# Optimization experiments

Hardware: AMD Instinct MI355X
Metric: run time of the kernel (lower is better)

Reference implementation:

```python
import jax, jax.numpy as jnp
import numpy as np

B, T, D, H = 4, 2048, 1024, 16
DH = D // H  # head dim = 64

def setup_inputs() -> dict:
    key = jax.random.key(0)
    k1, k2, k3, k4, k5, k6 = jax.random.split(key, 6)
    x = jax.random.normal(k1, (B, T, D), dtype=jnp.float32)
    mask = jax.random.randint(k2, (B, 1, 1, T), 0, 2, dtype=jnp.int32)
    # nn.Linear(out_dim, out_dim*3): weight stored here as [in, out]
    W_qkv = jax.random.normal(k3, (D, 3 * D), dtype=jnp.float32) * (1.0 / np.sqrt(D))
    b_qkv = jax.random.normal(k4, (3 * D,), dtype=jnp.float32) * 0.02
    W_out = jax.random.normal(k5, (D, D), dtype=jnp.float32) * (1.0 / np.sqrt(D))
    b_out = jax.random.normal(k6, (D,), dtype=jnp.float32) * 0.02
    return {"x": x, "mask": mask, "W_qkv": W_qkv, "b_qkv": b_qkv,
            "W_out": W_out, "b_out": b_out}

def reference(x, mask, W_qkv, b_qkv, W_out, b_out):
    # QKV projection: [B,T,3D]
    qkv = x @ W_qkv + b_qkv
    q, k, v = qkv[..., :D], qkv[..., D:2 * D], qkv[..., 2 * D:]
    # split heads -> [B,H,T,DH]
    def split(t):
        return t.reshape(B, T, H, DH).transpose(0, 2, 1, 3)
    q, k, v = split(q), split(k), split(v)
    # scaled dot-product attention (scale = sqrt(head_dim), per torch source)
    scores = jnp.einsum('bhqd,bhkd->bhqk', q, k) / jnp.sqrt(jnp.float32(DH))
    scores = jnp.where(mask == 0, jnp.float32(-1000.0), scores)
    weights = jax.nn.softmax(scores, axis=-1)  # dropout = identity (eval mode)
    out = jnp.einsum('bhqk,bhkd->bhqd', weights, v)
    out = out.transpose(0, 2, 1, 3).reshape(B, T, D)
    return out @ W_out + b_out
```

## Files before the change

### kernel.cpp

```cpp
#include <hip/hip_runtime.h>
#include <hip/hip_bf16.h>
#include <stdint.h>

#define B_  4
#define T_  2048
#define D_  1024
#define H_  16
#define DH_ 64

typedef _Float16 half8 __attribute__((ext_vector_type(8)));
typedef _Float16 half4 __attribute__((ext_vector_type(4)));
typedef __fp16   fp16x2 __attribute__((ext_vector_type(2)));
typedef float    f32x4 __attribute__((ext_vector_type(4)));

#define MFMA16(a, b, c) __builtin_amdgcn_mfma_f32_16x16x32_f16(a, b, c, 0, 0, 0)

__device__ static inline void gload_lds16(const void* g, void* l) {
  __builtin_amdgcn_global_load_lds(
      (const __attribute__((address_space(1))) void*)g,
      (__attribute__((address_space(3))) void*)l, 16, 0, 0);
}

__global__ __launch_bounds__(256)
void prep_all(const float* __restrict__ x, const int* __restrict__ mask,
              const float* __restrict__ wqkv, const float* __restrict__ wout,
              _Float16* __restrict__ xh, _Float16* __restrict__ mh,
              _Float16* __restrict__ wqkvt, _Float16* __restrict__ woutt) {
  __shared__ float tile[32][33];
  const int bid = blockIdx.x, t = threadIdx.x;
  if (bid < 2048) {
    const long n = (long)B_ * T_ * D_;
    long i = ((long)bid * 256 + t) * 4;
    const long stride = (long)2048 * 256 * 4;
    for (; i < n; i += stride) {
      float4 v = *(const float4*)(x + i);
      half4 hv;
      hv.x = (_Float16)v.x; hv.y = (_Float16)v.y; hv.z = (_Float16)v.z; hv.w = (_Float16)v.w;
      *(half4*)(xh + i) = hv;
    }
  } else if (bid < 6144) {
    const float* in;
    _Float16* out;
    int n0, k0, N;
    if (bid < 5120) {
      int id = bid - 2048;
      in = wqkv; out = wqkvt; N = 3 * D_;
      n0 = (id % 96) * 32; k0 = (id / 96) * 32;
    } else {
      int id = bid - 5120;
      in = wout; out = woutt; N = D_;
      n0 = (id % 32) * 32; k0 = (id / 32) * 32;
    }
    const int xx = t & 31, y = t >> 5;
    #pragma unroll
    for (int j = 0; j < 32; j += 8)
      tile[y + j][xx] = in[(long)(k0 + y + j) * N + n0 + xx];
    __syncthreads();
    #pragma unroll
    for (int j = 0; j < 32; j += 8)
      out[(long)(n0 + y + j) * D_ + k0 + xx] = (_Float16)tile[xx][y + j];
  } else {
    int i = (bid - 6144) * 256 + t;
    mh[i] = mask[i] ? (_Float16)1.0f : (_Float16)0.0f;
  }
}

template <int EPI>
__global__ __launch_bounds__(256, 2)
void mha_gemm2(const _Float16* __restrict__ A, const _Float16* __restrict__ Bt,
               const float* __restrict__ bias, const _Float16* __restrict__ mhp,
               _Float16* __restrict__ qo, _Float16* __restrict__ ko, _Float16* __restrict__ vo,
               float* __restrict__ co, int M, int N, int K, int gx) {
  __shared__ _Float16 shbuf[16384];
  _Float16* const As = shbuf;
  _Float16* const Bs = shbuf + 8192;
  const int t = threadIdx.x;
  const int l = t & 63;
  const int w = t >> 6;
  const int wr = w >> 1, wc = w & 1;

  const int cpx = gridDim.x >> 3;
  const int wg = (blockIdx.x & 7) * cpx + (blockIdx.x >> 3);
  const int m0 = (wg / gx) * 128, n0 = (wg % gx) * 128;

  const _Float16* ag[4];
  const _Float16* bg[4];
  #pragma unroll
  for (int j = 0; j < 4; ++j) {
    int c = j * 256 + t;
    int row = c >> 3, sub = c & 7;
    int s = (sub ^ (row & 7)) * 8;
    ag[j] = A  + (long)(m0 + row) * K + s;
    bg[j] = Bt + (long)(n0 + row) * K + s;
  }

  f32x4 acc[4][4];
  #pragma unroll
  for (int f = 0; f < 4; ++f)
    #pragma unroll
    for (int g = 0; g < 4; ++g) acc[f][g] = (f32x4){0.f, 0.f, 0.f, 0.f};

  const int hi = l >> 4;

  for (int k0 = 0; k0 < K; k0 += 64) {
    #pragma unroll
    for (int j = 0; j < 4; ++j) {
      gload_lds16(ag[j] + k0, &As[j * 2048 + w * 512]);
      gload_lds16(bg[j] + k0, &Bs[j * 2048 + w * 512]);
    }
    __syncthreads();
    half8 af[2][4], bf[2][4];
    #pragma unroll
    for (int kk = 0; kk < 2; ++kk)
      #pragma unroll
      for (int f = 0; f < 4; ++f) {
        int ra = wr * 64 + f * 16 + (l & 15);
        int rb = wc * 64 + f * 16 + (l & 15);
        af[kk][f] = *(const half8*)((const char*)As + ra * 128 +
                                    ((((kk << 2) | hi) ^ (ra & 7)) << 4));
        bf[kk][f] = *(const half8*)((const char*)Bs + rb * 128 +
                                    ((((kk << 2) | hi) ^ (rb & 7)) << 4));
      }
    #pragma unroll
    for (int kk = 0; kk < 2; ++kk)
      #pragma unroll
      for (int f = 0; f < 4; ++f)
        #pragma unroll
        for (int g = 0; g < 4; ++g)
          acc[f][g] = MFMA16(af[kk][f], bf[kk][g], acc[f][g]);
    __syncthreads();
  }

  if constexpr (EPI == 0) {
    if (n0 >= 2 * D_) {
      const int bb = m0 >> 11, m0t = m0 & 2047;
      #pragma unroll
      for (int g = 0; g < 4; ++g) {
        int colL = wc * 64 + g * 16 + (l & 15);
        float bv = bias[n0 + colL];
        int swz = (colL & 7) << 4;
        #pragma unroll
        for (int f = 0; f < 4; ++f) {
          int row0 = wr * 64 + f * 16 + hi * 4;
          half4 hv;
          #pragma unroll
          for (int r = 0; r < 4; ++r) {
            float mv = (float)mhp[bb * T_ + m0t + row0 + r];
            hv[r] = (_Float16)((acc[f][g][r] + bv) * mv);
          }
          *(half4*)&shbuf[colL * 128 + (row0 ^ swz)] = hv;
        }
      }
      __syncthreads();
      #pragma unroll
      for (int i = 0; i < 8; ++i) {
        int e = i * 256 + t;
        int colL = e >> 4, chunk = e & 15;
        int swz = (colL & 7) << 4;
        half8 v8 = *(const half8*)&shbuf[colL * 128 + ((chunk * 8) ^ swz)];
        int d = (n0 + colL) & 1023;
        int h2 = d >> 6, dh = d & 63;
        *(half8*)&vo[(((long)bb * H_ + h2) * DH_ + dh) * T_ + m0t + chunk * 8] = v8;
      }
    } else {
      #pragma unroll
      for (int g = 0; g < 4; ++g) {
        int j = n0 + wc * 64 + g * 16 + (l & 15);
        float bv = bias[j];
        int which = j >> 10;
        int d = j & 1023;
        int h = d >> 6, dh = d & 63;
        _Float16* base = which == 0 ? qo : ko;
        float sc = which == 0 ? 0.1803368801f : 1.0f;
        #pragma unroll
        for (int f = 0; f < 4; ++f) {
          int row0 = m0 + wr * 64 + f * 16 + ((l >> 4) << 2);
          #pragma unroll
          for (int r = 0; r < 4; ++r) {
            int row = row0 + r;
            int bb = row >> 11, tt = row & 2047;
            base[(((long)bb * H_ + h) * T_ + tt) * DH_ + dh] =
                (_Float16)((acc[f][g][r] + bv) * sc);
          }
        }
      }
    }
  } else {
    #pragma unroll
    for (int g = 0; g < 4; ++g) {
      int j = n0 + wc * 64 + g * 16 + (l & 15);
      float bv = bias[j];
      #pragma unroll
      for (int f = 0; f < 4; ++f) {
        int row0 = m0 + wr * 64 + f * 16 + ((l >> 4) << 2);
        #pragma unroll
        for (int r = 0; r < 4; ++r)
          co[(long)(row0 + r) * N + j] = acc[f][g][r] + bv;
      }
    }
  }
}

__global__ __launch_bounds__(128, 2)
void mha_attn7(const _Float16* __restrict__ Q, const _Float16* __restrict__ K,
               const _Float16* __restrict__ Vt, const _Float16* __restrict__ mh,
               _Float16* __restrict__ out) {
  __shared__ _Float16 Ksh[2][4096];
  __shared__ _Float16 Vsh[2][4096];
  const int t = threadIdx.x, l = t & 63, w = t >> 6;
  const int hi = l >> 4, q = l & 15;

  const int bid = blockIdx.x;
  const int idx = bid >> 3;
  const int bh = (bid & 7) * 8 + (idx >> 4);
  const int qt = idx & 15;
  const int b = bh >> 4, h = bh & 15;
  const long base = (long)bh * (T_ * DH_);
  const int qb = qt * 128 + w * 64;

  half8 qf[4][2];
  #pragma unroll
  for (int G = 0; G < 4; ++G) {
    qf[G][0] = *(const half8*)(Q + base + (long)(qb + G * 16 + q) * DH_ + hi * 8);
    qf[G][1] = *(const half8*)(Q + base + (long)(qb + G * 16 + q) * DH_ + hi * 8 + 32);
  }

  const _Float16* ks[4];
  const _Float16* vs[4];
  #pragma unroll
  for (int j = 0; j < 4; ++j) {
    int c = w * 256 + j * 64 + l;
    int row = c >> 3, sub = c & 7;
    int s = (sub ^ ((row & 7) ^ ((row >> 2) & 7))) * 8;
    ks[j] = K  + base + row * DH_ + s;
    vs[j] = Vt + base + (long)row * T_ + s;
  }

  int kcb[4];
  #pragma unroll
  for (int g = 0; g < 4; ++g) {
    int kr = (g >> 1) * 32 + (q >> 2) * 8 + (g & 1) * 4 + (q & 3);
    int sw = (kr & 7) ^ ((kr >> 2) & 7);
    kcb[g] = kr * 128 + ((hi * 16) ^ (sw << 4));
  }
  int vcb[4];
  #pragma unroll
  for (int o = 0; o < 4; ++o) {
    int vr = o * 16 + q;
    int sw = (vr & 7) ^ ((vr >> 2) & 7);
    vcb[o] = vr * 128 + ((hi * 16) ^ (sw << 4));
  }

  const _Float16* mrow = mh + b * T_ + hi * 8;

  f32x4 acc[4][4], accD[4];
  #pragma unroll
  for (int G = 0; G < 4; ++G) {
    accD[G] = (f32x4){0.f, 0.f, 0.f, 0.f};
    #pragma unroll
    for (int o = 0; o < 4; ++o) acc[G][o] = (f32x4){0.f, 0.f, 0.f, 0.f};
  }

#define STAGEKV(BI, TT) do {                                                 \
    _Pragma("unroll")                                                        \
    for (int j = 0; j < 4; ++j) {                                            \
      gload_lds16(ks[j] + (TT) * (64 * DH_), &Ksh[BI][w * 2048 + j * 512]);  \
      gload_lds16(vs[j] + (TT) * 64,         &Vsh[BI][w * 2048 + j * 512]);  \
    }                                                                        \
  } while (0)

  STAGEKV(0, 0);
  __syncthreads();

  for (int kt = 0; kt < T_ / 64; ++kt) {
    const int bi = kt & 1;
    if (kt + 1 < T_ / 64) STAGEKV(bi ^ 1, kt + 1);

    const half8 mf0 = *(const half8*)(mrow + kt * 64);
    const half8 mf1 = *(const half8*)(mrow + kt * 64 + 32);

    const char* kbb = (const char*)Ksh[bi];
    const char* vbb = (const char*)Vsh[bi];
    half8 kf[4][2];
    #pragma unroll
    for (int g = 0; g < 4; ++g) {
      kf[g][0] = *(const half8*)(kbb + kcb[g]);
      kf[g][1] = *(const half8*)(kbb + (kcb[g] ^ 64));
    }
    half8 vf[4][2];
    #pragma unroll
    for (int o = 0; o < 4; ++o) {
      vf[o][0] = *(const half8*)(vbb + vcb[o]);
      vf[o][1] = *(const half8*)(vbb + (vcb[o] ^ 64));
    }

    #pragma unroll
    for (int G = 0; G < 4; ++G) {
      __builtin_amdgcn_s_setprio(1);
      f32x4 z[4];
      #pragma unroll
      for (int g = 0; g < 4; ++g) {
        f32x4 zz = (f32x4){0.f, 0.f, 0.f, 0.f};
        zz = MFMA16(kf[g][0], qf[G][0], zz);
        z[g] = MFMA16(kf[g][1], qf[G][1], zz);
      }
      __builtin_amdgcn_s_setprio(0);
      union { fp16x2 h2[4]; half8 h8; } u0, u1;
      #pragma unroll
      for (int i = 0; i < 2; ++i) {
        u0.h2[i]     = __builtin_amdgcn_cvt_pkrtz(__builtin_amdgcn_exp2f(z[0][2*i]),
                                                  __builtin_amdgcn_exp2f(z[0][2*i+1]));
        u0.h2[2 + i] = __builtin_amdgcn_cvt_pkrtz(__builtin_amdgcn_exp2f(z[1][2*i]),
                                                  __builtin_amdgcn_exp2f(z[1][2*i+1]));
        u1.h2[i]     = __builtin_amdgcn_cvt_pkrtz(__builtin_amdgcn_exp2f(z[2][2*i]),
                                                  __builtin_amdgcn_exp2f(z[2][2*i+1]));
        u1.h2[2 + i] = __builtin_amdgcn_cvt_pkrtz(__builtin_amdgcn_exp2f(z[3][2*i]),
                                                  __builtin_amdgcn_exp2f(z[3][2*i+1]));
      }
      __builtin_amdgcn_s_setprio(1);
      accD[G] = MFMA16(u0.h8, mf0, accD[G]);
      accD[G] = MFMA16(u1.h8, mf1, accD[G]);
      #pragma unroll
      for (int o = 0; o < 4; ++o) {
        acc[G][o] = MFMA16(u0.h8, vf[o][0], acc[G][o]);
        acc[G][o] = MFMA16(u1.h8, vf[o][1], acc[G][o]);
      }
      __builtin_amdgcn_s_setprio(0);
    }
    __syncthreads();
  }
#undef STAGEKV

  #pragma unroll
  for (int G = 0; G < 4; ++G)
    #pragma unroll
    for (int r = 0; r < 4; ++r) {
      float inv = __builtin_amdgcn_rcpf(accD[G][r]);
      int trow = qb + G * 16 + hi * 4 + r;
      #pragma unroll
      for (int o = 0; o < 4; ++o)
        out[((long)b * T_ + trow) * D_ + h * DH_ + o * 16 + q] =
            (_Float16)(acc[G][o][r] * inv);
    }
}

extern "C" void kernel_launch(void* const* d_in, const int* in_sizes, int n_in,
                              void* d_out, int out_size, void* d_ws, size_t ws_size,
                              hipStream_t stream) {
  const float* x    = (const float*)d_in[0];
  const int*   mask = (const int*)d_in[1];
  const float* wqkv = (const float*)d_in[2];
  const float* bqkv = (const float*)d_in[3];
  const float* wout = (const float*)d_in[4];
  const float* bout = (const float*)d_in[5];
  float* out = (float*)d_out;

  _Float16* ws = (_Float16*)d_ws;
  const long nX = (long)B_ * T_ * D_;
  _Float16* xh    = ws;
  _Float16* wqkvt = xh + nX;
  _Float16* woutt = wqkvt + (long)D_ * 3 * D_;
  _Float16* mh    = woutt + (long)D_ * D_;
  _Float16* Qb    = woutt + (long)D_ * D_ + 16384;
  _Float16* Kb    = Qb + nX;
  _Float16* Vtg   = Kb + nX;
  _Float16* attnh = Vtg + nX;

  prep_all<<<6176, 256, 0, stream>>>(x, mask, wqkv, wout, xh, mh, wqkvt, woutt);

  mha_gemm2<0><<<1536, 256, 0, stream>>>(
      xh, wqkvt, bqkv, mh, Qb, Kb, Vtg, nullptr, B_ * T_, 3 * D_, D_, 24);

  mha_attn7<<<1024, 128, 0, stream>>>(Qb, Kb, Vtg, mh, attnh);

  mha_gemm2<1><<<512, 256, 0, stream>>>(
      attnh, woutt, bout, nullptr, nullptr, nullptr, nullptr, out, B_ * T_, D_, D_, 8);
}
```

Before: 172.5 us.

## Restructure GEMMs into 256x128 tiles with 3-stage async LDS pipeline

Replaces the 128x128, 256-thread GEMM with a 256x128 tile on 512 threads (8 waves). The K loop becomes a fully unrolled triple-buffered pipeline: global-to-LDS loads are issued three stages ahead and gated with explicit vmcnt waits and raw barriers. MFMA sections run at raised wave priority. The aim is to hide global load latency behind MFMA work and get more reuse per A/B load. In exchange it uses 144KB of LDS per block, so only one block fits per CU, and K is now hard-coded to D.

```diff
diff --git a/kernel.cpp b/kernel.cpp
--- a/kernel.cpp
+++ b/kernel.cpp
@@ -66,33 +66,40 @@
 }
 
 template <int EPI>
-__global__ __launch_bounds__(256, 2)
-void mha_gemm2(const _Float16* __restrict__ A, const _Float16* __restrict__ Bt,
+__global__ __launch_bounds__(512)
+void mha_gemm9(const _Float16* __restrict__ A, const _Float16* __restrict__ Bt,
                const float* __restrict__ bias, const _Float16* __restrict__ mhp,
-               _Float16* __restrict__ qo, _Float16* __restrict__ ko, _Float16* __restrict__ vo,
-               float* __restrict__ co, int M, int N, int K, int gx) {
-  __shared__ _Float16 shbuf[16384];
-  _Float16* const As = shbuf;
-  _Float16* const Bs = shbuf + 8192;
-  const int t = threadIdx.x;
-  const int l = t & 63;
-  const int w = t >> 6;
-  const int wr = w >> 1, wc = w & 1;
+               _Float16* __restrict__ qo, _Float16* __restrict__ ko,
+               _Float16* __restrict__ vo, float* __restrict__ co,
+               int Nout, int gx) {
+  __shared__ _Float16 shbuf[73728];
+  const int tid = threadIdx.x;
+  const int l = tid & 63, w = tid >> 6;
+  const int wm = w >> 1, wn = w & 1;
+  const int hi = l >> 4, q = l & 15;
+  const int K = D_;
 
   const int cpx = gridDim.x >> 3;
   const int wg = (blockIdx.x & 7) * cpx + (blockIdx.x >> 3);
-  const int m0 = (wg / gx) * 128, n0 = (wg % gx) * 128;
-
-  const _Float16* ag[4];
-  const _Float16* bg[4];
-  #pragma unroll
-  for (int j = 0; j < 4; ++j) {
-    int c = j * 256 + t;
-    int row = c >> 3, sub = c & 7;
-    int s = (sub ^ (row & 7)) * 8;
-    ag[j] = A  + (long)(m0 + row) * K + s;
-    bg[j] = Bt + (long)(n0 + row) * K + s;
-  }
+  const int m0 = (wg / gx) * 256, n0 = (wg % gx) * 128;
+  const int bb = m0 >> 11, m0t = m0 & 2047;
+
+  const int srow = tid >> 3, ssub = tid & 7;
+  const int ssw = ssub ^ (srow & 7);
+  const _Float16* a0 = A  + (long)(m0 + srow) * K + ssw * 8;
+  const _Float16* b0 = Bt + (long)(n0 + srow) * K + ssw * 8;
+  _Float16* lA = shbuf + tid * 8;
+  _Float16* lB = shbuf + 49152 + tid * 8;
+  const long joff = (long)64 * K;
+
+#define STG(S, T) do {                                                       \
+    _Pragma("unroll")                                                        \
+    for (int j = 0; j < 4; ++j)                                              \
+      gload_lds16(a0 + (T) * 64 + j * joff, lA + (S) * 16384 + j * 4096);    \
+    _Pragma("unroll")                                                        \
+    for (int j = 0; j < 2; ++j)                                              \
+      gload_lds16(b0 + (T) * 64 + j * joff, lB + (S) * 8192 + j * 4096);     \
+  } while (0)
 
   f32x4 acc[4][4];
   #pragma unroll
@@ -100,27 +107,42 @@
     #pragma unroll
     for (int g = 0; g < 4; ++g) acc[f][g] = (f32x4){0.f, 0.f, 0.f, 0.f};
 
-  const int hi = l >> 4;
-
-  for (int k0 = 0; k0 < K; k0 += 64) {
-    #pragma unroll
-    for (int j = 0; j < 4; ++j) {
-      gload_lds16(ag[j] + k0, &As[j * 2048 + w * 512]);
-      gload_lds16(bg[j] + k0, &Bs[j * 2048 + w * 512]);
-    }
-    __syncthreads();
+  const char* const Ab = (const char*)shbuf;
+  const char* const Bb = (const char*)(shbuf + 49152);
+
+  STG(0, 0); STG(1, 1); STG(2, 2);
+
+  #pragma unroll
+  for (int t = 0; t < 16; ++t) {
+    const int S = t % 3;
+    if (t <= 13)      asm volatile("s_waitcnt vmcnt(12)" ::: "memory");
+    else if (t == 14) asm volatile("s_waitcnt vmcnt(6)" ::: "memory");
+    else              asm volatile("s_waitcnt vmcnt(0)" ::: "memory");
+    __builtin_amdgcn_s_barrier();
+
     half8 af[2][4], bf[2][4];
     #pragma unroll
-    for (int kk = 0; kk < 2; ++kk)
+    for (int kk = 0; kk < 2; ++kk) {
       #pragma unroll
       for (int f = 0; f < 4; ++f) {
-        int ra = wr * 64 + f * 16 + (l & 15);
-        int rb = wc * 64 + f * 16 + (l & 15);
-        af[kk][f] = *(const half8*)((const char*)As + ra * 128 +
+        int ra = wm * 64 + f * 16 + q;
+        af[kk][f] = *(const half8*)(Ab + S * 32768 + ra * 128 +
                                     ((((kk << 2) | hi) ^ (ra & 7)) << 4));
-        bf[kk][f] = *(const half8*)((const char*)Bs + rb * 128 +
+      }
+      #pragma unroll
+      for (int g = 0; g < 4; ++g) {
+        int rb = wn * 64 + g * 16 + q;
+        bf[kk][g] = *(const half8*)(Bb + S * 16384 + rb * 128 +
                                     ((((kk << 2) | hi) ^ (rb & 7)) << 4));
       }
+    }
+    asm volatile("s_waitcnt lgkmcnt(0)" ::: "memory");
+    __builtin_amdgcn_sched_barrier(0);
+    __builtin_amdgcn_s_barrier();
+    __builtin_amdgcn_sched_barrier(0);
+    if (t + 3 < 16) STG(S, t + 3);
+
+    __builtin_amdgcn_s_setprio(1);
     #pragma unroll
     for (int kk = 0; kk < 2; ++kk)
       #pragma unroll
@@ -128,74 +150,72 @@
         #pragma unroll
         for (int g = 0; g < 4; ++g)
           acc[f][g] = MFMA16(af[kk][f], bf[kk][g], acc[f][g]);
-    __syncthreads();
-  }
+    __builtin_amdgcn_s_setprio(0);
+  }
+#undef STG
+  __syncthreads();
 
   if constexpr (EPI == 0) {
-    if (n0 >= 2 * D_) {
-      const int bb = m0 >> 11, m0t = m0 & 2047;
+    const int which = n0 >> 10;
+    if (which == 2) {
       #pragma unroll
       for (int g = 0; g < 4; ++g) {
-        int colL = wc * 64 + g * 16 + (l & 15);
+        int colL = wn * 64 + g * 16 + q;
         float bv = bias[n0 + colL];
-        int swz = (colL & 7) << 4;
+        int swz = (colL & 7) << 3;
         #pragma unroll
         for (int f = 0; f < 4; ++f) {
-          int row0 = wr * 64 + f * 16 + hi * 4;
+          int row0 = wm * 64 + f * 16 + hi * 4;
           half4 hv;
           #pragma unroll
           for (int r = 0; r < 4; ++r) {
             float mv = (float)mhp[bb * T_ + m0t + row0 + r];
             hv[r] = (_Float16)((acc[f][g][r] + bv) * mv);
           }
-          *(half4*)&shbuf[colL * 128 + (row0 ^ swz)] = hv;
+          *(half4*)&shbuf[colL * 256 + (row0 ^ swz)] = hv;
         }
       }
       __syncthreads();
       #pragma unroll
-      for (int i = 0; i < 8; ++i) {
-        int e = i * 256 + t;
-        int colL = e >> 4, chunk = e & 15;
-        int swz = (colL & 7) << 4;
-        half8 v8 = *(const half8*)&shbuf[colL * 128 + ((chunk * 8) ^ swz)];
+      for (int it = 0; it < 8; ++it) {
+        int e = it * 512 + tid;
+        int colL = e >> 5, chunk = e & 31;
+        int swz = (colL & 7) << 3;
+        half8 v8 = *(const half8*)&shbuf[colL * 256 + ((chunk * 8) ^ swz)];
         int d = (n0 + colL) & 1023;
         int h2 = d >> 6, dh = d & 63;
         *(half8*)&vo[(((long)bb * H_ + h2) * DH_ + dh) * T_ + m0t + chunk * 8] = v8;
       }
     } else {
+      _Float16* base = which == 0 ? qo : ko;
+      const float sc = which == 0 ? 0.1803368801f : 1.0f;
       #pragma unroll
       for (int g = 0; g < 4; ++g) {
-        int j = n0 + wc * 64 + g * 16 + (l & 15);
+        int j = n0 + wn * 64 + g * 16 + q;
         float bv = bias[j];
-        int which = j >> 10;
         int d = j & 1023;
         int h = d >> 6, dh = d & 63;
-        _Float16* base = which == 0 ? qo : ko;
-        float sc = which == 0 ? 0.1803368801f : 1.0f;
         #pragma unroll
         for (int f = 0; f < 4; ++f) {
-          int row0 = m0 + wr * 64 + f * 16 + ((l >> 4) << 2);
+          int rowL = m0t + wm * 64 + f * 16 + hi * 4;
           #pragma unroll
-          for (int r = 0; r < 4; ++r) {
-            int row = row0 + r;
-            int bb = row >> 11, tt = row & 2047;
-            base[(((long)bb * H_ + h) * T_ + tt) * DH_ + dh] =
+          for (int r = 0; r < 4; ++r)
+            base[(((long)bb * H_ + h) * T_ + rowL + r) * DH_ + dh] =
                 (_Float16)((acc[f][g][r] + bv) * sc);
-          }
         }
       }
     }
   } else {
     #pragma unroll
     for (int g = 0; g < 4; ++g) {
-      int j = n0 + wc * 64 + g * 16 + (l & 15);
+      int j = n0 + wn * 64 + g * 16 + q;
       float bv = bias[j];
       #pragma unroll
       for (int f = 0; f < 4; ++f) {
-        int row0 = m0 + wr * 64 + f * 16 + ((l >> 4) << 2);
+        int row0 = m0 + wm * 64 + f * 16 + hi * 4;
         #pragma unroll
         for (int r = 0; r < 4; ++r)
-          co[(long)(row0 + r) * N + j] = acc[f][g][r] + bv;
+          co[(long)(row0 + r) * Nout + j] = acc[f][g][r] + bv;
       }
     }
   }
@@ -368,11 +388,11 @@
 
   prep_all<<<6176, 256, 0, stream>>>(x, mask, wqkv, wout, xh, mh, wqkvt, woutt);
 
-  mha_gemm2<0><<<1536, 256, 0, stream>>>(
-      xh, wqkvt, bqkv, mh, Qb, Kb, Vtg, nullptr, B_ * T_, 3 * D_, D_, 24);
+  mha_gemm9<0><<<768, 512, 0, stream>>>(
+      xh, wqkvt, bqkv, mh, Qb, Kb, Vtg, nullptr, 3 * D_, 24);
 
   mha_attn7<<<1024, 128, 0, stream>>>(Qb, Kb, Vtg, mh, attnh);
 
-  mha_gemm2<1><<<512, 256, 0, stream>>>(
-      attnh, woutt, bout, nullptr, nullptr, nullptr, nullptr, out, B_ * T_, D_, D_, 8);
-}
+  mha_gemm9<1><<<256, 512, 0, stream>>>(
+      attnh, woutt, bout, nullptr, nullptr, nullptr, nullptr, out, D_, 8);
+}
```

Result: slower. 180.9 us (+4.9%).
